# Performance work log

Measured on AMD Instinct MI355X. Metric: run time of the kernel, lower is better.

Reference implementation:

```python
import jax, jax.numpy as jnp
import numpy as np


def _oneplus(x):
    return 1.0 + jax.nn.softplus(x)


def _content(mem, keys, beta):
    # mem: [B,A,M], keys: [B,K,M], beta: [B,K] -> weights [B,K,A]
    eps = 1e-6
    dot = jnp.einsum('bam,bkm->bka', mem, keys)
    mn = jnp.linalg.norm(mem, axis=-1)   # [B,A]
    kn = jnp.linalg.norm(keys, axis=-1)  # [B,K]
    cos = dot / (kn[:, :, None] * mn[:, None, :] + eps)
    return jax.nn.softmax(beta[:, :, None] * cos, axis=-1)


def setup_inputs():
    key = jax.random.key(0)
    ks = jax.random.split(key, 20)
    B, I, H, O, A, M, R = 16, 256, 512, 256, 1024, 64, 4
    IF = R * M + R + M + 1 + M + M + R + 2 + 3 * R  # 471
    def lin(k, fi, fo):
        return jax.random.normal(k, (fi, fo)) / np.sqrt(fi)
    eye = jnp.eye(A)
    return dict(
        x=jax.random.normal(ks[0], (B, I)),
        h_prev=jax.random.normal(ks[1], (B, H)) * 0.1,
        c_prev=jax.random.normal(ks[2], (B, H)) * 0.1,
        mem_prev=jax.random.normal(ks[3], (B, A, M)) * 0.1,
        rw_prev=jax.nn.softmax(jax.random.normal(ks[4], (B, R, A)), axis=-1),
        ww_prev=jax.nn.softmax(jax.random.normal(ks[5], (B, A)), axis=-1),
        usage_prev=jax.random.uniform(ks[6], (B, A)),
        prec_prev=jax.nn.softmax(jax.random.normal(ks[7], (B, A)), axis=-1),
        link_prev=jax.random.uniform(ks[8], (B, A, A)) * 1e-3 * (1.0 - eye),
        rv_prev=jax.random.normal(ks[9], (B, R * M)) * 0.1,
        Wx=lin(ks[10], I + R * M, 4 * H),
        Wh=lin(ks[11], H, 4 * H),
        b_lstm=jnp.zeros((4 * H,)),
        W_hid=lin(ks[12], H, O),
        b_hid=jnp.zeros((O,)),
        W_if=lin(ks[13], H, IF),
        b_if=jnp.zeros((IF,)),
        W_rd=lin(ks[14], R * M, O),
        b_rd=jnp.zeros((O,)),
    )


def reference(x, h_prev, c_prev, mem_prev, rw_prev, ww_prev, usage_prev, prec_prev,
              link_prev, rv_prev, Wx, Wh, b_lstm, W_hid, b_hid, W_if, b_if, W_rd, b_rd):
    B, R, A = rw_prev.shape
    M = mem_prev.shape[-1]
    # --- controller LSTM over [input, prev read vectors] ---
    z = jnp.concatenate([x, rv_prev], axis=-1) @ Wx + h_prev @ Wh + b_lstm
    i, f, g, o = jnp.split(z, 4, axis=-1)
    c = jax.nn.sigmoid(f) * c_prev + jax.nn.sigmoid(i) * jnp.tanh(g)
    h = jax.nn.sigmoid(o) * jnp.tanh(c)
    out_hidden = h @ W_hid + b_hid
    iface = h @ W_if + b_if
    # --- split interface vector ---
    p = 0
    k_r = iface[:, p:p + R * M].reshape(B, R, M); p += R * M
    beta_r = _oneplus(iface[:, p:p + R]); p += R
    k_w = iface[:, p:p + M]; p += M
    beta_w = _oneplus(iface[:, p:p + 1]); p += 1
    erase = jax.nn.sigmoid(iface[:, p:p + M]); p += M
    write_v = iface[:, p:p + M]; p += M
    free = jax.nn.sigmoid(iface[:, p:p + R]); p += R
    g_a = jax.nn.sigmoid(iface[:, p:p + 1]); p += 1
    g_w = jax.nn.sigmoid(iface[:, p:p + 1]); p += 1
    pi = jax.nn.softmax(iface[:, p:p + 3 * R].reshape(B, R, 3), axis=-1)
    # --- usage / retention ---
    psi = jnp.prod(1.0 - free[:, :, None] * rw_prev, axis=1)  # [B,A]
    usage = (usage_prev + ww_prev - usage_prev * ww_prev) * psi
    # --- allocation weighting via sorted usage ---
    idx = jnp.argsort(usage, axis=-1)
    su = jnp.take_along_axis(usage, idx, axis=-1)
    cp = jnp.cumprod(su, axis=-1)
    cp_excl = jnp.concatenate([jnp.ones_like(cp[:, :1]), cp[:, :-1]], axis=-1)
    a_sorted = (1.0 - su) * cp_excl
    alloc = jnp.take_along_axis(a_sorted, jnp.argsort(idx, axis=-1), axis=-1)
    # --- write weighting + memory edit ---
    c_w = _content(mem_prev, k_w[:, None, :], beta_w)[:, 0]  # [B,A]
    ww = g_w * (g_a * alloc + (1.0 - g_a) * c_w)
    mem = mem_prev * (1.0 - ww[:, :, None] * erase[:, None, :]) + ww[:, :, None] * write_v[:, None, :]
    # --- temporal link / precedence ---
    link = (1.0 - ww[:, :, None] - ww[:, None, :]) * link_prev + ww[:, :, None] * prec_prev[:, None, :]
    link = link * (1.0 - jnp.eye(A, dtype=link.dtype))
    prec = (1.0 - jnp.sum(ww, axis=-1, keepdims=True)) * prec_prev + ww
    # --- read weighting: backward / content / forward modes ---
    fwd_w = jnp.einsum('bij,brj->bri', link, rw_prev)
    bwd_w = jnp.einsum('bji,brj->bri', link, rw_prev)
    c_r = _content(mem, k_r, beta_r)
    w_r = pi[..., 0:1] * bwd_w + pi[..., 1:2] * c_r + pi[..., 2:3] * fwd_w
    rv = jnp.einsum('bra,bam->brm', w_r, mem).reshape(B, R * M)
    return out_hidden + rv @ W_rd + b_rd
```

## Files before the change

kernel.cpp:

```cpp
#include <hip/hip_runtime.h>
#include <math.h>


__device__ __forceinline__ float sigf(float x){ return 1.0f/(1.0f+expf(-x)); }
__device__ __forceinline__ float softplusf(float x){ return fmaxf(x,0.0f)+log1pf(expf(-fabsf(x))); }

__global__ __launch_bounds__(256) void k_lstm_part(const float* __restrict__ x,
    const float* __restrict__ rv, const float* __restrict__ hp,
    const float* __restrict__ Wx, const float* __restrict__ Wh,
    float* __restrict__ zpart){
  __shared__ float inp[8][64];
  int ct = blockIdx.x, kt = blockIdx.y, bg = blockIdx.z, t = threadIdx.x;
  for (int i = t; i < 512; i += 256){
    int bb = i >> 6, kk = i & 63;
    int k = kt*64 + kk, b = bg*8 + bb;
    float v = (k < 256) ? x[b*256+k] : (k < 512) ? rv[b*256 + k-256] : hp[b*512 + k-512];
    inp[bb][kk] = v;
  }
  __syncthreads();
  int col = ct*256 + t;
  float acc[8];
  #pragma unroll
  for (int bb = 0; bb < 8; ++bb) acc[bb] = 0.0f;
  for (int kk = 0; kk < 64; ++kk){
    int k = kt*64 + kk;
    float w = (k < 512) ? Wx[(long)k*2048 + col] : Wh[(long)(k-512)*2048 + col];
    #pragma unroll
    for (int bb = 0; bb < 8; ++bb) acc[bb] += inp[bb][kk]*w;
  }
  #pragma unroll
  for (int bb = 0; bb < 8; ++bb)
    zpart[((long)kt*16 + bg*8 + bb)*2048 + col] = acc[bb];
}

__global__ void k_lstm_fin(const float* __restrict__ zpart, const float* __restrict__ bl,
                           const float* __restrict__ cp, float* __restrict__ h_ws){
  int jt = blockIdx.x, b = blockIdx.y, j = jt*128 + threadIdx.x;
  float zi = bl[j], zf = bl[512+j], zg = bl[1024+j], zo = bl[1536+j];
  for (int kt = 0; kt < 16; ++kt){
    const float* zp = zpart + ((long)kt*16 + b)*2048;
    zi += zp[j]; zf += zp[512+j]; zg += zp[1024+j]; zo += zp[1536+j];
  }
  float c = sigf(zf)*cp[b*512+j] + sigf(zi)*tanhf(zg);
  h_ws[b*512+j] = sigf(zo)*tanhf(c);
}

__global__ __launch_bounds__(256) void k_iface_part(const float* __restrict__ h_ws,
    const float* __restrict__ W_if, const float* __restrict__ W_hid,
    float* __restrict__ ifpart){
  __shared__ float hh[8][32];
  int ct = blockIdx.x, kt = blockIdx.y, bg = blockIdx.z, t = threadIdx.x;
  {
    int bb = t >> 5, kk = t & 31;
    hh[bb][kk] = h_ws[(bg*8 + bb)*512 + kt*32 + kk];
  }
  __syncthreads();
  int col = ct*256 + t;
  float acc[8];
  #pragma unroll
  for (int bb = 0; bb < 8; ++bb) acc[bb] = 0.0f;
  if (col < 727){
    for (int kk = 0; kk < 32; ++kk){
      int k = kt*32 + kk;
      float w = (col < 471) ? W_if[(long)k*471 + col] : W_hid[(long)k*256 + (col-471)];
      #pragma unroll
      for (int bb = 0; bb < 8; ++bb) acc[bb] += hh[bb][kk]*w;
    }
    #pragma unroll
    for (int bb = 0; bb < 8; ++bb)
      ifpart[((long)kt*16 + bg*8 + bb)*768 + col] = acc[bb];
  }
}

__global__ void k_iface_fin(const float* __restrict__ ifpart, const float* __restrict__ b_if,
                            const float* __restrict__ b_hid, float* __restrict__ ifr_ws,
                            float* __restrict__ outh_ws){
  int b = blockIdx.x, t = threadIdx.x;
  if (t >= 727) return;
  float s = (t < 471) ? b_if[t] : b_hid[t-471];
  for (int kt = 0; kt < 16; ++kt) s += ifpart[((long)kt*16 + b)*768 + t];
  if (t < 471) ifr_ws[b*512 + t] = s;
  else         outh_ws[b*256 + (t-471)] = s;
}

__global__ void k_act_alloc(const float* __restrict__ ifr_ws, const float* __restrict__ rw_prev,
                            const float* __restrict__ ww_prev, const float* __restrict__ usage_prev,
                            float* __restrict__ ifa_ws, float* __restrict__ alloc_ws){
  __shared__ float sifa[480];
  __shared__ unsigned long long keys[1024];
  __shared__ float wtot[16];
  int b = blockIdx.x, t = threadIdx.x;
  int lane = t & 63, wid = t >> 6;
  const float* ifr = ifr_ws + b*512;
  if (t < 471){
    float v = ifr[t], o = v;
    if ((t >= 256 && t < 260) || t == 324) o = 1.0f + softplusf(v);
    else if ((t >= 325 && t < 389) || (t >= 453 && t < 459)) o = sigf(v);
    sifa[t] = o;
  }
  __syncthreads();
  if (t < 4){
    float p0 = ifr[459+t*3+0], p1 = ifr[459+t*3+1], p2 = ifr[459+t*3+2];
    float mx = fmaxf(p0, fmaxf(p1,p2));
    float e0 = expf(p0-mx), e1 = expf(p1-mx), e2 = expf(p2-mx);
    float s = e0+e1+e2;
    sifa[459+t*3+0]=e0/s; sifa[459+t*3+1]=e1/s; sifa[459+t*3+2]=e2/s;
  }
  __syncthreads();
  if (t < 471) ifa_ws[b*512 + t] = sifa[t];
  float f0 = sifa[453], f1 = sifa[454], f2 = sifa[455], f3 = sifa[456];
  float psi = (1.f - f0*rw_prev[(long)(b*4+0)*1024 + t])
            * (1.f - f1*rw_prev[(long)(b*4+1)*1024 + t])
            * (1.f - f2*rw_prev[(long)(b*4+2)*1024 + t])
            * (1.f - f3*rw_prev[(long)(b*4+3)*1024 + t]);
  float uu = usage_prev[b*1024+t], w = ww_prev[b*1024+t];
  float uval = (uu + w - uu*w) * psi;
  unsigned int ub = __float_as_uint(uval);
  unsigned int k32 = ub ^ (((int)ub >> 31) | 0x80000000u);
  unsigned long long key = ((unsigned long long)k32 << 32) | (unsigned int)t;
  for (int kk2 = 2; kk2 <= 1024; kk2 <<= 1){
    for (int j = kk2 >> 1; j > 0; j >>= 1){
      unsigned long long other;
      if (j >= 64){
        keys[t] = key;
        __syncthreads();
        other = keys[t ^ j];
        __syncthreads();
      } else {
        other = __shfl_xor(key, j);
      }
      bool up = ((t & kk2) == 0);
      bool keepMin = (((t & j) == 0) == up);
      if (keepMin ? (other < key) : (other > key)) key = other;
    }
  }
  unsigned int hk = (unsigned int)(key >> 32);
  unsigned int ob = (hk & 0x80000000u) ? (hk ^ 0x80000000u) : ~hk;
  float su = __uint_as_float(ob);
  int oi = (int)(key & 1023u);
  float s = su;
  #pragma unroll
  for (int off = 1; off < 64; off <<= 1){
    float v = __shfl_up(s, off);
    if (lane >= off) s *= v;
  }
  if (lane == 63) wtot[wid] = s;
  __syncthreads();
  float wpre = 1.0f;
  for (int w2 = 0; w2 < wid; ++w2) wpre *= wtot[w2];
  float ex = __shfl_up(s, 1);
  if (lane == 0) ex = 1.0f;
  float cpe = ex * wpre;
  alloc_ws[b*1024 + oi] = (1.0f - su) * cpe;
}

__global__ __launch_bounds__(512) void k_wscore(const float* __restrict__ mem_prev,
    const float* __restrict__ ifa_ws, float* __restrict__ wsc_ws){
  int at = blockIdx.x, b = blockIdx.y;
  int t = threadIdx.x, w = t >> 6, m = t & 63;
  const float* ifa = ifa_ws + b*512;
  float kwm = ifa[260+m], beta = ifa[324];
  float knsq = kwm*kwm;
  for (int o = 32; o > 0; o >>= 1) knsq += __shfl_xor(knsq, o);
  float kn = sqrtf(knsq);
  for (int rr = 0; rr < 8; ++rr){
    int a = at*64 + w*8 + rr;
    float v = mem_prev[((long)b*1024+a)*64+m];
    float d = v*kwm, sq = v*v;
    for (int o = 32; o > 0; o >>= 1){ d += __shfl_xor(d,o); sq += __shfl_xor(sq,o); }
    if (m == 0) wsc_ws[b*1024+a] = beta*d/(kn*sqrtf(sq)+1e-6f);
  }
}

__global__ void k_cw_ww(const float* __restrict__ wsc_ws, const float* __restrict__ ifa_ws,
                        const float* __restrict__ alloc_ws, const float* __restrict__ rw_prev,
                        float* __restrict__ ww_ws, float* __restrict__ e_ws){
  __shared__ float wred[16]; __shared__ float wred2[16];
  int b = blockIdx.x, t = threadIdx.x, lane = t & 63, wid = t >> 6;
  const float* ifa = ifa_ws + b*512;
  float g_a = ifa[457], g_w = ifa[458];
  float sc = wsc_ws[b*1024+t];
  float m = sc;
  for (int o = 32; o > 0; o >>= 1) m = fmaxf(m, __shfl_xor(m, o));
  if (lane == 0) wred[wid] = m;
  __syncthreads();
  float mx = wred[0];
  #pragma unroll
  for (int i = 1; i < 16; ++i) mx = fmaxf(mx, wred[i]);
  float e = expf(sc - mx);
  float ssum = e;
  for (int o = 32; o > 0; o >>= 1) ssum += __shfl_xor(ssum, o);
  if (lane == 0) wred2[wid] = ssum;
  __syncthreads();
  float tot = 0.0f;
  #pragma unroll
  for (int i = 0; i < 16; ++i) tot += wred2[i];
  float cw = e / tot;
  float ww = g_w*(g_a*alloc_ws[b*1024+t] + (1.0f-g_a)*cw);
  ww_ws[b*1024+t] = ww;
  #pragma unroll
  for (int r = 0; r < 4; ++r)
    e_ws[(long)(b*4+r)*1024 + t] = ww * rw_prev[(long)(b*4+r)*1024 + t];
}

__global__ __launch_bounds__(512) void k_score(const float* __restrict__ mem_prev,
    const float* __restrict__ ww_ws, const float* __restrict__ ifa_ws,
    float* __restrict__ mnorm_ws, float* __restrict__ rdot_ws){
  int at = blockIdx.x, b = blockIdx.y;
  int t = threadIdx.x, w = t >> 6, m = t & 63;
  const float* ifa = ifa_ws + b*512;
  float er = ifa[325+m], wv = ifa[389+m];
  float k0 = ifa[m], k1 = ifa[64+m], k2 = ifa[128+m], k3 = ifa[192+m];
  for (int rr = 0; rr < 8; ++rr){
    int a = at*64 + w*8 + rr;
    float ww = ww_ws[b*1024+a];
    float v = mem_prev[((long)b*1024+a)*64+m]*(1.0f - ww*er) + ww*wv;
    float sq = v*v, d0 = v*k0, d1 = v*k1, d2 = v*k2, d3 = v*k3;
    for (int o = 32; o > 0; o >>= 1){
      sq += __shfl_xor(sq,o); d0 += __shfl_xor(d0,o); d1 += __shfl_xor(d1,o);
      d2 += __shfl_xor(d2,o); d3 += __shfl_xor(d3,o);
    }
    if (m == 0){
      mnorm_ws[b*1024+a] = sqrtf(sq);
      rdot_ws[(long)(b*4+0)*1024+a] = d0; rdot_ws[(long)(b*4+1)*1024+a] = d1;
      rdot_ws[(long)(b*4+2)*1024+a] = d2; rdot_ws[(long)(b*4+3)*1024+a] = d3;
    }
  }
}

__global__ __launch_bounds__(256) void k_linkfb(const float* __restrict__ link_prev,
    const float* __restrict__ rw_prev, const float* __restrict__ e_ws,
    const float* __restrict__ prec_prev, const float* __restrict__ ww_ws,
    float* __restrict__ fwd_part, float* __restrict__ bwd_part){
  __shared__ float Lt[64][68];
  int band = blockIdx.x, ct = blockIdx.y, b = blockIdx.z, t = threadIdx.x;
  int r = t >> 6, lane = t & 63;
  int ru = __builtin_amdgcn_readfirstlane(r);
  const float4* L4 = (const float4*)link_prev;
  #pragma unroll
  for (int q = 0; q < 4; ++q){
    int idx = t + 256*q;
    int row = idx >> 4, c4 = idx & 15;
    float4 v = L4[((long)b << 18) + (long)(band*64+row)*256 + ct*16 + c4];
    *(float4*)&Lt[row][c4*4] = v;
  }
  const float* aJ = rw_prev + (long)(b*4+ru)*1024 + ct*64;
  const float* eJ = e_ws    + (long)(b*4+ru)*1024 + ct*64;
  const float* aI = rw_prev + (long)(b*4+ru)*1024 + band*64;
  const float* eI = e_ws    + (long)(b*4+ru)*1024 + band*64;
  float pv = prec_prev[b*1024 + ct*64 + lane] * aJ[lane];
  float wvs = eI[lane];
  for (int o = 32; o > 0; o >>= 1){ pv += __shfl_xor(pv,o); wvs += __shfl_xor(wvs,o); }
  float wwi = ww_ws[b*1024 + band*64 + lane];
  float wwc = ww_ws[b*1024 + ct*64 + lane];
  float pc  = prec_prev[b*1024 + ct*64 + lane];
  __syncthreads();
  float A1 = 0.0f, A2 = 0.0f;
  for (int jc = 0; jc < 64; jc += 4){
    float4 Lv = *(const float4*)&Lt[lane][jc];
    A1 += Lv.x*aJ[jc] + Lv.y*aJ[jc+1] + Lv.z*aJ[jc+2] + Lv.w*aJ[jc+3];
    A2 += Lv.x*eJ[jc] + Lv.y*eJ[jc+1] + Lv.z*eJ[jc+2] + Lv.w*eJ[jc+3];
  }
  float facc = (1.0f - wwi)*A1 - A2 + wwi*pv;
  float B1 = 0.0f, B2 = 0.0f;
  for (int rowl = 0; rowl < 64; ++rowl){
    float Lv = Lt[rowl][lane];
    B1 += Lv * aI[rowl];
    B2 += Lv * eI[rowl];
  }
  float bacc = (1.0f - wwc)*B1 - B2 + pc*wvs;
  if (band == ct){
    float D = ((1.0f - 2.0f*wwi)*Lt[lane][lane] + wwi*pc)*aJ[lane];
    facc -= D;
    bacc -= D;
  }
  fwd_part[(long)ct*65536 + (long)(b*4+r)*1024 + band*64 + lane] = facc;
  bwd_part[(long)band*65536 + (long)(b*4+r)*1024 + ct*64 + lane] = bacc;
}

__global__ void k_read(const float* __restrict__ rdot_ws, const float* __restrict__ mnorm_ws,
                       const float* __restrict__ ifa_ws, const float* __restrict__ fwd_part,
                       const float* __restrict__ bwd_part, const float* __restrict__ mem_prev,
                       const float* __restrict__ ww_ws, float* __restrict__ rv_ws){
  __shared__ float red[1024]; __shared__ float wrs[1024]; __shared__ float wwsh[1024];
  __shared__ float par[1]; __shared__ float wred[16]; __shared__ float wred2[16];
  int r = blockIdx.x, b = blockIdx.y, t = threadIdx.x;
  int lane = t & 63, wid = t >> 6;
  const float* ifa = ifa_ws + b*512;
  long base = (long)(b*4+r)*1024 + t;
  float fsum = 0.0f, bsum = 0.0f;
  #pragma unroll
  for (int c = 0; c < 16; ++c){
    fsum += fwd_part[(long)c*65536 + base];
    bsum += bwd_part[(long)c*65536 + base];
  }
  if (t < 64){
    float v = ifa[r*64+t];
    float sq = v*v;
    for (int o = 32; o > 0; o >>= 1) sq += __shfl_xor(sq, o);
    if (t == 0) par[0] = sqrtf(sq);
  }
  wwsh[t] = ww_ws[b*1024+t];
  __syncthreads();
  float kn = par[0], beta = ifa[256 + r];
  float sc = beta * rdot_ws[base] / (kn*mnorm_ws[b*1024+t] + 1e-6f);
  float m = sc;
  for (int o = 32; o > 0; o >>= 1) m = fmaxf(m, __shfl_xor(m, o));
  if (lane == 0) wred[wid] = m;
  __syncthreads();
  float mx = wred[0];
  #pragma unroll
  for (int i = 1; i < 16; ++i) mx = fmaxf(mx, wred[i]);
  float e = expf(sc - mx);
  float s = e;
  for (int o = 32; o > 0; o >>= 1) s += __shfl_xor(s, o);
  if (lane == 0) wred2[wid] = s;
  __syncthreads();
  float tot = 0.0f;
  #pragma unroll
  for (int i = 0; i < 16; ++i) tot += wred2[i];
  float cr = e / tot;
  float p0 = ifa[459+3*r], p1 = ifa[460+3*r], p2 = ifa[461+3*r];
  wrs[t] = p0*bsum + p1*cr + p2*fsum;
  __syncthreads();
  int mm = t & 63, ch = t >> 6;
  float er = ifa[325+mm], wv = ifa[389+mm];
  float acc = 0;
  for (int q = 0; q < 64; ++q){
    int a = ch*64 + q;
    float w = wwsh[a];
    float v = mem_prev[((long)b*1024 + a)*64 + mm]*(1.0f - w*er) + w*wv;
    acc += wrs[a]*v;
  }
  red[ch*64 + mm] = acc;
  __syncthreads();
  if (t < 64){
    float s2 = 0;
    for (int c2 = 0; c2 < 16; ++c2) s2 += red[c2*64 + t];
    rv_ws[(b*4+r)*64 + t] = s2;
  }
}

__global__ void k_out(const float* __restrict__ outh_ws, const float* __restrict__ rv_ws,
                      const float* __restrict__ W_rd, const float* __restrict__ b_rd,
                      float* __restrict__ out){
  __shared__ float rvs[256]; __shared__ float part[4][256];
  int b = blockIdx.x, t = threadIdx.x;
  int o = t & 255, kq = t >> 8;
  if (t < 256) rvs[t] = rv_ws[b*256 + t];
  __syncthreads();
  float acc = 0.0f;
  for (int q = kq*64; q < kq*64 + 64; ++q) acc += rvs[q]*W_rd[(long)q*256 + o];
  part[kq][o] = acc;
  __syncthreads();
  if (t < 256)
    out[b*256+t] = outh_ws[b*256+t] + b_rd[t] + part[0][t] + part[1][t] + part[2][t] + part[3][t];
}

extern "C" void kernel_launch(void* const* d_in, const int* in_sizes, int n_in,
                              void* d_out, int out_size, void* d_ws, size_t ws_size,
                              hipStream_t stream){
  const float* x          = (const float*)d_in[0];
  const float* h_prev     = (const float*)d_in[1];
  const float* c_prev     = (const float*)d_in[2];
  const float* mem_prev   = (const float*)d_in[3];
  const float* rw_prev    = (const float*)d_in[4];
  const float* ww_prev    = (const float*)d_in[5];
  const float* usage_prev = (const float*)d_in[6];
  const float* prec_prev  = (const float*)d_in[7];
  const float* link_prev  = (const float*)d_in[8];
  const float* rv_prev    = (const float*)d_in[9];
  const float* Wx         = (const float*)d_in[10];
  const float* Wh         = (const float*)d_in[11];
  const float* b_lstm     = (const float*)d_in[12];
  const float* W_hid      = (const float*)d_in[13];
  const float* b_hid      = (const float*)d_in[14];
  const float* W_if       = (const float*)d_in[15];
  const float* b_if       = (const float*)d_in[16];
  const float* W_rd       = (const float*)d_in[17];
  const float* b_rd       = (const float*)d_in[18];
  float* out = (float*)d_out;

  float* ws = (float*)d_ws;
  float* h_ws     = ws + 0;
  float* ifr_ws   = ws + 8192;
  float* ifa_ws   = ws + 16384;
  float* outh_ws  = ws + 24576;
  float* alloc_ws = ws + 28672;
  float* ww_ws    = ws + 45056;
  float* mnorm_ws = ws + 61440;
  float* wsc_ws   = ws + 77824;
  float* rv_ws    = ws + 94208;
  float* fwd_ws   = ws + 98304;
  float* bwd_ws   = ws + 163840;
  float* rdot_ws  = ws + 229376;
  float* e_ws     = ws + 294912;
  float* zpart    = ws + 360448;
  float* ifpart   = ws + 884736;
  float* fwd_part = ws + 1081344;
  float* bwd_part = ws + 2129920;
  (void)fwd_ws; (void)bwd_ws;

  k_lstm_part<<<dim3(8,16,2),256,0,stream>>>(x, rv_prev, h_prev, Wx, Wh, zpart);
  k_lstm_fin<<<dim3(4,16),128,0,stream>>>(zpart, b_lstm, c_prev, h_ws);
  k_iface_part<<<dim3(3,16,2),256,0,stream>>>(h_ws, W_if, W_hid, ifpart);
  k_iface_fin<<<16,768,0,stream>>>(ifpart, b_if, b_hid, ifr_ws, outh_ws);
  k_act_alloc<<<16,1024,0,stream>>>(ifr_ws, rw_prev, ww_prev, usage_prev, ifa_ws, alloc_ws);
  k_wscore<<<dim3(16,16),512,0,stream>>>(mem_prev, ifa_ws, wsc_ws);
  k_cw_ww<<<16,1024,0,stream>>>(wsc_ws, ifa_ws, alloc_ws, rw_prev, ww_ws, e_ws);
  k_score<<<dim3(16,16),512,0,stream>>>(mem_prev, ww_ws, ifa_ws, mnorm_ws, rdot_ws);
  k_linkfb<<<dim3(16,16,16),256,0,stream>>>(link_prev, rw_prev, e_ws, prec_prev, ww_ws,
                                            fwd_part, bwd_part);
  k_read<<<dim3(4,16),1024,0,stream>>>(rdot_ws, mnorm_ws, ifa_ws, fwd_part, bwd_part,
                                       mem_prev, ww_ws, rv_ws);
  k_out<<<16,1024,0,stream>>>(outh_ws, rv_ws, W_rd, b_rd, out);
}
```

Before: 229.5 us.

## Fuse iface reduction into activation kernel and merge score with link kernel

The LSTM and interface GEMV kernels now handle all 16 batch rows per block, which halves their grid and reads each weight once instead of twice. The interface partial-sum reduction is folded into the activation/allocation kernel, removing one launch and the ifr round trip. The memory-score kernel and the link forward/backward kernel are merged into one launch, with block ranges split by blockIdx, so they can run concurrently. The cost is fewer blocks in the GEMV stages (less parallelism) and a heterogeneous merged grid.

Result: no change. 229.4 us (-0.0%).

```diff
diff --git a/kernel.cpp b/kernel.cpp
--- a/kernel.cpp
+++ b/kernel.cpp
@@ -9,28 +9,30 @@
     const float* __restrict__ rv, const float* __restrict__ hp,
     const float* __restrict__ Wx, const float* __restrict__ Wh,
     float* __restrict__ zpart){
-  __shared__ float inp[8][64];
-  int ct = blockIdx.x, kt = blockIdx.y, bg = blockIdx.z, t = threadIdx.x;
-  for (int i = t; i < 512; i += 256){
+  __shared__ float inp[16][64];
+  int ct = blockIdx.x, kt = blockIdx.y, t = threadIdx.x;
+  #pragma unroll
+  for (int q = 0; q < 4; ++q){
+    int i = t + 256*q;
     int bb = i >> 6, kk = i & 63;
-    int k = kt*64 + kk, b = bg*8 + bb;
-    float v = (k < 256) ? x[b*256+k] : (k < 512) ? rv[b*256 + k-256] : hp[b*512 + k-512];
+    int k = kt*64 + kk;
+    float v = (k < 256) ? x[bb*256+k] : (k < 512) ? rv[bb*256 + k-256] : hp[bb*512 + k-512];
     inp[bb][kk] = v;
   }
   __syncthreads();
   int col = ct*256 + t;
-  float acc[8];
-  #pragma unroll
-  for (int bb = 0; bb < 8; ++bb) acc[bb] = 0.0f;
+  float acc[16];
+  #pragma unroll
+  for (int bb = 0; bb < 16; ++bb) acc[bb] = 0.0f;
   for (int kk = 0; kk < 64; ++kk){
     int k = kt*64 + kk;
     float w = (k < 512) ? Wx[(long)k*2048 + col] : Wh[(long)(k-512)*2048 + col];
     #pragma unroll
-    for (int bb = 0; bb < 8; ++bb) acc[bb] += inp[bb][kk]*w;
-  }
-  #pragma unroll
-  for (int bb = 0; bb < 8; ++bb)
-    zpart[((long)kt*16 + bg*8 + bb)*2048 + col] = acc[bb];
+    for (int bb = 0; bb < 16; ++bb) acc[bb] += inp[bb][kk]*w;
+  }
+  #pragma unroll
+  for (int bb = 0; bb < 16; ++bb)
+    zpart[((long)kt*16 + bb)*2048 + col] = acc[bb];
 }
 
 __global__ void k_lstm_fin(const float* __restrict__ zpart, const float* __restrict__ bl,
@@ -48,59 +50,60 @@
 __global__ __launch_bounds__(256) void k_iface_part(const float* __restrict__ h_ws,
     const float* __restrict__ W_if, const float* __restrict__ W_hid,
     float* __restrict__ ifpart){
-  __shared__ float hh[8][32];
-  int ct = blockIdx.x, kt = blockIdx.y, bg = blockIdx.z, t = threadIdx.x;
-  {
-    int bb = t >> 5, kk = t & 31;
-    hh[bb][kk] = h_ws[(bg*8 + bb)*512 + kt*32 + kk];
+  __shared__ float hh[16][32];
+  int ct = blockIdx.x, kt = blockIdx.y, t = threadIdx.x;
+  #pragma unroll
+  for (int q = 0; q < 2; ++q){
+    int i = t + 256*q;
+    int bb = i >> 5, kk = i & 31;
+    hh[bb][kk] = h_ws[bb*512 + kt*32 + kk];
   }
   __syncthreads();
   int col = ct*256 + t;
-  float acc[8];
-  #pragma unroll
-  for (int bb = 0; bb < 8; ++bb) acc[bb] = 0.0f;
+  float acc[16];
+  #pragma unroll
+  for (int bb = 0; bb < 16; ++bb) acc[bb] = 0.0f;
   if (col < 727){
     for (int kk = 0; kk < 32; ++kk){
       int k = kt*32 + kk;
       float w = (col < 471) ? W_if[(long)k*471 + col] : W_hid[(long)k*256 + (col-471)];
       #pragma unroll
-      for (int bb = 0; bb < 8; ++bb) acc[bb] += hh[bb][kk]*w;
+      for (int bb = 0; bb < 16; ++bb) acc[bb] += hh[bb][kk]*w;
     }
     #pragma unroll
-    for (int bb = 0; bb < 8; ++bb)
-      ifpart[((long)kt*16 + bg*8 + bb)*768 + col] = acc[bb];
-  }
-}
-
-__global__ void k_iface_fin(const float* __restrict__ ifpart, const float* __restrict__ b_if,
-                            const float* __restrict__ b_hid, float* __restrict__ ifr_ws,
-                            float* __restrict__ outh_ws){
-  int b = blockIdx.x, t = threadIdx.x;
-  if (t >= 727) return;
-  float s = (t < 471) ? b_if[t] : b_hid[t-471];
-  for (int kt = 0; kt < 16; ++kt) s += ifpart[((long)kt*16 + b)*768 + t];
-  if (t < 471) ifr_ws[b*512 + t] = s;
-  else         outh_ws[b*256 + (t-471)] = s;
-}
-
-__global__ void k_act_alloc(const float* __restrict__ ifr_ws, const float* __restrict__ rw_prev,
+    for (int bb = 0; bb < 16; ++bb)
+      ifpart[((long)kt*16 + bb)*768 + col] = acc[bb];
+  }
+}
+
+__global__ __launch_bounds__(1024) void k_actfa(const float* __restrict__ ifpart,
+                            const float* __restrict__ b_if, const float* __restrict__ b_hid,
+                            const float* __restrict__ rw_prev,
                             const float* __restrict__ ww_prev, const float* __restrict__ usage_prev,
+                            float* __restrict__ outh_ws,
                             float* __restrict__ ifa_ws, float* __restrict__ alloc_ws){
+  __shared__ float sraw[480];
   __shared__ float sifa[480];
   __shared__ unsigned long long keys[1024];
   __shared__ float wtot[16];
   int b = blockIdx.x, t = threadIdx.x;
   int lane = t & 63, wid = t >> 6;
-  const float* ifr = ifr_ws + b*512;
-  if (t < 471){
-    float v = ifr[t], o = v;
+  if (t < 727){
+    float s = (t < 471) ? b_if[t] : b_hid[t-471];
+    #pragma unroll
+    for (int kt = 0; kt < 16; ++kt) s += ifpart[((long)kt*16 + b)*768 + t];
+    if (t < 471) sraw[t] = s;
+    else         outh_ws[b*256 + (t-471)] = s;
+  }
+  __syncthreads();
+  if (t < 459){
+    float v = sraw[t], o = v;
     if ((t >= 256 && t < 260) || t == 324) o = 1.0f + softplusf(v);
     else if ((t >= 325 && t < 389) || (t >= 453 && t < 459)) o = sigf(v);
     sifa[t] = o;
   }
-  __syncthreads();
   if (t < 4){
-    float p0 = ifr[459+t*3+0], p1 = ifr[459+t*3+1], p2 = ifr[459+t*3+2];
+    float p0 = sraw[459+t*3+0], p1 = sraw[459+t*3+1], p2 = sraw[459+t*3+2];
     float mx = fmaxf(p0, fmaxf(p1,p2));
     float e0 = expf(p0-mx), e1 = expf(p1-mx), e2 = expf(p2-mx);
     float s = e0+e1+e2;
@@ -203,37 +206,39 @@
     e_ws[(long)(b*4+r)*1024 + t] = ww * rw_prev[(long)(b*4+r)*1024 + t];
 }
 
-__global__ __launch_bounds__(512) void k_score(const float* __restrict__ mem_prev,
+__global__ __launch_bounds__(256) void k_slfb(const float* __restrict__ mem_prev,
     const float* __restrict__ ww_ws, const float* __restrict__ ifa_ws,
-    float* __restrict__ mnorm_ws, float* __restrict__ rdot_ws){
-  int at = blockIdx.x, b = blockIdx.y;
-  int t = threadIdx.x, w = t >> 6, m = t & 63;
-  const float* ifa = ifa_ws + b*512;
-  float er = ifa[325+m], wv = ifa[389+m];
-  float k0 = ifa[m], k1 = ifa[64+m], k2 = ifa[128+m], k3 = ifa[192+m];
-  for (int rr = 0; rr < 8; ++rr){
-    int a = at*64 + w*8 + rr;
-    float ww = ww_ws[b*1024+a];
-    float v = mem_prev[((long)b*1024+a)*64+m]*(1.0f - ww*er) + ww*wv;
-    float sq = v*v, d0 = v*k0, d1 = v*k1, d2 = v*k2, d3 = v*k3;
-    for (int o = 32; o > 0; o >>= 1){
-      sq += __shfl_xor(sq,o); d0 += __shfl_xor(d0,o); d1 += __shfl_xor(d1,o);
-      d2 += __shfl_xor(d2,o); d3 += __shfl_xor(d3,o);
-    }
-    if (m == 0){
-      mnorm_ws[b*1024+a] = sqrtf(sq);
-      rdot_ws[(long)(b*4+0)*1024+a] = d0; rdot_ws[(long)(b*4+1)*1024+a] = d1;
-      rdot_ws[(long)(b*4+2)*1024+a] = d2; rdot_ws[(long)(b*4+3)*1024+a] = d3;
-    }
-  }
-}
-
-__global__ __launch_bounds__(256) void k_linkfb(const float* __restrict__ link_prev,
-    const float* __restrict__ rw_prev, const float* __restrict__ e_ws,
-    const float* __restrict__ prec_prev, const float* __restrict__ ww_ws,
+    float* __restrict__ mnorm_ws, float* __restrict__ rdot_ws,
+    const float* __restrict__ link_prev, const float* __restrict__ rw_prev,
+    const float* __restrict__ e_ws, const float* __restrict__ prec_prev,
     float* __restrict__ fwd_part, float* __restrict__ bwd_part){
   __shared__ float Lt[64][68];
-  int band = blockIdx.x, ct = blockIdx.y, b = blockIdx.z, t = threadIdx.x;
+  int bid = blockIdx.x, t = threadIdx.x;
+  if (bid < 256){
+    int at = bid & 15, b = bid >> 4;
+    int w = t >> 6, m = t & 63;
+    const float* ifa = ifa_ws + b*512;
+    float er = ifa[325+m], wv = ifa[389+m];
+    float k0 = ifa[m], k1 = ifa[64+m], k2 = ifa[128+m], k3 = ifa[192+m];
+    for (int rr = 0; rr < 16; ++rr){
+      int a = at*64 + w*16 + rr;
+      float ww = ww_ws[b*1024+a];
+      float v = mem_prev[((long)b*1024+a)*64+m]*(1.0f - ww*er) + ww*wv;
+      float sq = v*v, d0 = v*k0, d1 = v*k1, d2 = v*k2, d3 = v*k3;
+      for (int o = 32; o > 0; o >>= 1){
+        sq += __shfl_xor(sq,o); d0 += __shfl_xor(d0,o); d1 += __shfl_xor(d1,o);
+        d2 += __shfl_xor(d2,o); d3 += __shfl_xor(d3,o);
+      }
+      if (m == 0){
+        mnorm_ws[b*1024+a] = sqrtf(sq);
+        rdot_ws[(long)(b*4+0)*1024+a] = d0; rdot_ws[(long)(b*4+1)*1024+a] = d1;
+        rdot_ws[(long)(b*4+2)*1024+a] = d2; rdot_ws[(long)(b*4+3)*1024+a] = d3;
+      }
+    }
+    return;
+  }
+  int lb = bid - 256;
+  int band = lb & 15, ct = (lb >> 4) & 15, b = lb >> 8;
   int r = t >> 6, lane = t & 63;
   int ru = __builtin_amdgcn_readfirstlane(r);
   const float4* L4 = (const float4*)link_prev;
@@ -399,18 +404,17 @@
   float* ifpart   = ws + 884736;
   float* fwd_part = ws + 1081344;
   float* bwd_part = ws + 2129920;
-  (void)fwd_ws; (void)bwd_ws;
-
-  k_lstm_part<<<dim3(8,16,2),256,0,stream>>>(x, rv_prev, h_prev, Wx, Wh, zpart);
+  (void)ifr_ws; (void)fwd_ws; (void)bwd_ws;
+
+  k_lstm_part<<<dim3(8,16),256,0,stream>>>(x, rv_prev, h_prev, Wx, Wh, zpart);
   k_lstm_fin<<<dim3(4,16),128,0,stream>>>(zpart, b_lstm, c_prev, h_ws);
-  k_iface_part<<<dim3(3,16,2),256,0,stream>>>(h_ws, W_if, W_hid, ifpart);
-  k_iface_fin<<<16,768,0,stream>>>(ifpart, b_if, b_hid, ifr_ws, outh_ws);
-  k_act_alloc<<<16,1024,0,stream>>>(ifr_ws, rw_prev, ww_prev, usage_prev, ifa_ws, alloc_ws);
+  k_iface_part<<<dim3(3,16),256,0,stream>>>(h_ws, W_if, W_hid, ifpart);
+  k_actfa<<<16,1024,0,stream>>>(ifpart, b_if, b_hid, rw_prev, ww_prev, usage_prev,
+                                outh_ws, ifa_ws, alloc_ws);
   k_wscore<<<dim3(16,16),512,0,stream>>>(mem_prev, ifa_ws, wsc_ws);
   k_cw_ww<<<16,1024,0,stream>>>(wsc_ws, ifa_ws, alloc_ws, rw_prev, ww_ws, e_ws);
-  k_score<<<dim3(16,16),512,0,stream>>>(mem_prev, ww_ws, ifa_ws, mnorm_ws, rdot_ws);
-  k_linkfb<<<dim3(16,16,16),256,0,stream>>>(link_prev, rw_prev, e_ws, prec_prev, ww_ws,
-                                            fwd_part, bwd_part);
+  k_slfb<<<4352,256,0,stream>>>(mem_prev, ww_ws, ifa_ws, mnorm_ws, rdot_ws,
+                                link_prev, rw_prev, e_ws, prec_prev, fwd_part, bwd_part);
   k_read<<<dim3(4,16),1024,0,stream>>>(rdot_ws, mnorm_ws, ifa_ws, fwd_part, bwd_part,
                                        mem_prev, ww_ws, rv_ws);
   k_out<<<16,1024,0,stream>>>(outh_ws, rv_ws, W_rd, b_rd, out);
```
